# Kernel optimization log

Measured on AMD Instinct MI355X. Metric: run time of the kernel, lower is better.

Reference implementation:

```python
import jax, jax.numpy as jnp
import numpy as np

L_SEG, M_CHEB, MODES1, MODES2 = 4, 8, 16, 16


def _cft(signals, t_coords, f_points, L, M):
    # signals: [N, C, n] real; returns (real, imag) each [N, C, F]
    n = signals.shape[-1]
    seg_len = 1.0 / L
    starts = jnp.linspace(0.0, 1.0, L + 1)[:-1]                      # [L]
    k = jnp.arange(M, dtype=jnp.float32)
    nodes = -jnp.cos((2.0 * k + 1.0) * jnp.pi / (2.0 * M))           # [M]
    T = jnp.cos(k[:, None] * jnp.arccos(nodes)[None, :])             # [M(k), M(m)]
    w_prime = f_points * (2.0 * jnp.pi * (seg_len / 2.0))            # [F]
    angle = nodes[:, None] * w_prime[None, :]                        # [M, F]
    # quad weights (index k is reused as node index m downstream, as in original)
    Wr = (T @ jnp.cos(angle)) * (seg_len / 2.0)                      # [M, F]
    Wi = (T @ (-jnp.sin(angle))) * (seg_len / 2.0)                   # [M, F] (sign = -1, forward)
    # chebyshev sample points for all segments at once
    t_seg = starts[:, None] + (seg_len / 2.0) * (nodes[None, :] + 1.0)   # [L, M]
    right = jnp.clip(jnp.searchsorted(t_coords, t_seg), 0, n - 1)
    left = jnp.clip(right - 1, 0, n - 1)
    tl, tr = t_coords[left], t_coords[right]
    denom = jnp.where(tr - tl < 1e-8, 1.0, tr - tl)
    wr = (t_seg - tl) / denom
    wl = 1.0 - wr
    seg_sig = wl * signals[..., left] + wr * signals[..., right]     # [N, C, L, M]
    Sr = jnp.einsum('nclm,mf->nclf', seg_sig, Wr)
    Si = jnp.einsum('nclm,mf->nclf', seg_sig, Wi)
    phase = -2.0 * jnp.pi * starts[:, None] * f_points[None, :]      # [L, F]
    cr, ci = jnp.cos(phase), jnp.sin(phase)
    real = jnp.sum(Sr * cr - Si * ci, axis=2)
    imag = jnp.sum(Sr * ci + Si * cr, axis=2)
    return real, imag


def _cft2d(x, m1, m2, L, M):
    B, C, H, W = x.shape
    tw = jnp.linspace(0.0, 1.0, W)
    fw = jnp.fft.rfftfreq(W, d=1.0 / W)[:m2].astype(jnp.float32)
    xr = x.transpose(0, 2, 1, 3).reshape(B * H, C, W)
    r, i = _cft(xr, tw, fw, L, M)                                    # [B*H, C, m2]
    r = r.reshape(B, H, C, m2).transpose(0, 2, 1, 3)                 # [B, C, H, m2]
    i = i.reshape(B, H, C, m2).transpose(0, 2, 1, 3)
    th = jnp.linspace(0.0, 1.0, H)
    fh = jnp.fft.fftfreq(H, d=1.0 / H).astype(jnp.float32)
    hidx = np.concatenate([np.arange(0, m1 // 2), np.arange(H - (m1 - m1 // 2), H)])
    fsel = fh[hidx]
    rh = r.transpose(0, 3, 1, 2).reshape(B * m2, C, H)
    ih = i.transpose(0, 3, 1, 2).reshape(B * m2, C, H)
    rr, ri = _cft(rh, th, fsel, L, M)
    ir, ii = _cft(ih, th, fsel, L, M)
    real = (rr - ii).reshape(B, m2, C, m1).transpose(0, 2, 3, 1)     # [B, C, m1, m2]
    imag = (ri + ir).reshape(B, m2, C, m1).transpose(0, 2, 3, 1)
    return real, imag


def setup_inputs() -> dict:
    key = jax.random.key(0)
    ks = jax.random.split(key, 6)
    B, C, O, H, W = 32, 64, 64, 128, 128
    m1, m2 = MODES1, MODES2
    scale = 1.0 / (C * O)
    x = jax.random.normal(ks[0], (B, C, H, W), jnp.float32)
    w1 = scale * jax.random.uniform(ks[1], (C, O, m1, m2, 2), jnp.float32)
    w2 = scale * jax.random.uniform(ks[2], (C, O, m1, m2, 2), jnp.float32)
    d_in = C * (m1 // 4) * (m2 // 4) * 2
    hid = (C + O) * 2
    lin1_w = jax.random.normal(ks[3], (d_in, hid), jnp.float32) * 0.02
    lin1_b = jnp.zeros((hid,), jnp.float32)
    lin2_w = jax.random.normal(ks[4], (hid, O), jnp.float32) * 0.02
    lin2_b = jnp.zeros((O,), jnp.float32)
    return dict(x=x, w1=w1, w2=w2, lin1_w=lin1_w, lin1_b=lin1_b, lin2_w=lin2_w, lin2_b=lin2_b)


def reference(x, w1, w2, lin1_w, lin1_b, lin2_w, lin2_b):
    m1, m2 = MODES1, MODES2
    B, C, H, W = x.shape
    O = w1.shape[1]
    # FNO spectral conv
    xf = jnp.fft.rfft2(x)                                            # [B, C, H, W//2+1]
    w1c = w1[..., 0] + 1j * w1[..., 1]
    w2c = w2[..., 0] + 1j * w2[..., 1]
    out_ft = jnp.zeros((B, O, H, W // 2 + 1), jnp.complex64)
    out_ft = out_ft.at[:, :, :m1, :m2].set(
        jnp.einsum('bixy,ioxy->boxy', xf[:, :, :m1, :m2], w1c))
    out_ft = out_ft.at[:, :, H - m1:, :m2].set(
        jnp.einsum('bixy,ioxy->boxy', xf[:, :, H - m1:, :m2], w2c))
    x_fno = jnp.fft.irfft2(out_ft, s=(H, W))
    # Chebyshev-quadrature CFT correction path
    cr, ci = _cft2d(x, m1 // 4, m2 // 4, L_SEG, M_CHEB)              # [B, C, m1//4, m2//4]
    flat = jnp.stack([cr, ci], axis=-1).reshape(B, -1)               # view_as_real + flatten(1)
    h = jax.nn.gelu(flat @ lin1_w + lin1_b, approximate=False)
    corr = h @ lin2_w + lin2_b                                       # [B, O]
    return x_fno + corr[:, :, None, None]
```

## Files before the change

kernel.cpp:

```cpp
#include <hip/hip_runtime.h>
#include <math.h>

#define PI_F 3.14159265358979323846f
#define TWO_PI_F 6.28318530717958647692f

constexpr int Bn = 32, Cn = 64, On = 64, Hn = 128, Wn = 128;

constexpr size_t WSO_FLAT  = 0;
constexpr size_t WSO_CORR  = 65536;
constexpr size_t WSO_HS    = 67584;
constexpr size_t WSO_BIG   = 81920;
constexpr size_t SZ_QTR    = (size_t)2097152;
constexpr size_t WSO_XF    = WSO_BIG + SZ_QTR;
constexpr size_t WSO_OUTFT = WSO_BIG + 4 * SZ_QTR;

struct Tabs {
  float ktw[128][40];
  float cfth[128][8];
};

constexpr double D_PI = 3.14159265358979323846;

constexpr double d_red(double x) {
  while (x >  D_PI) x -= 2.0 * D_PI;
  while (x < -D_PI) x += 2.0 * D_PI;
  return x;
}
constexpr double d_sin(double x) {
  x = d_red(x);
  double x2 = x * x, t = x, s = x;
  for (int n = 1; n <= 10; n++) { t *= -x2 / (double)((2 * n) * (2 * n + 1)); s += t; }
  return s;
}
constexpr double d_cos(double x) {
  x = d_red(x);
  double x2 = x * x, t = 1.0, s = 1.0;
  for (int n = 1; n <= 10; n++) { t *= -x2 / (double)((2 * n - 1) * (2 * n)); s += t; }
  return s;
}

constexpr Tabs make_tabs() {
  Tabs T{};
  double twc[128] = {}, tws[128] = {};
  for (int r = 0; r < 128; r++) {
    double a = 2.0 * D_PI * (double)r / 128.0;
    twc[r] = d_cos(a); tws[r] = d_sin(a);
  }
  for (int kx = 0; kx < 16; kx++)
    for (int w = 0; w < 128; w++) {
      int r = (kx * w) & 127;
      T.ktw[w][2 * kx]     = (float)twc[r];
      T.ktw[w][2 * kx + 1] = (float)(-tws[r]);
    }
  double node[8] = {}, theta[8] = {};
  for (int m = 0; m < 8; m++) { theta[m] = (2.0 * m + 1.0) * D_PI / 16.0; node[m] = -d_cos(theta[m]); }
  double Tch[8][8] = {};
  for (int k = 0; k < 8; k++)
    for (int m = 0; m < 8; m++) Tch[k][m] = d_cos((double)k * (D_PI - theta[m]));
  int LE[4][8] = {}, RI[4][8] = {};
  float WL[4][8] = {}, WR[4][8] = {};
  for (int l = 0; l < 4; l++)
    for (int m = 0; m < 8; m++) {
      float tseg = (float)(0.25 * (double)l + 0.125 * (node[m] + 1.0));
      int ri = (int)(tseg * 127.0f) - 2; if (ri < 0) ri = 0;
      while (ri < 127 && ((float)ri * (1.0f / 127.0f)) < tseg) ri++;
      int le = ri - 1; if (le < 0) le = 0;
      float tl = (float)le * (1.0f / 127.0f), tr = (float)ri * (1.0f / 127.0f);
      float den = (tr - tl < 1e-8f) ? 1.0f : (tr - tl);
      float wr = (tseg - tl) / den;
      LE[l][m] = le; RI[l][m] = ri; WR[l][m] = wr; WL[l][m] = 1.0f - wr;
    }
  for (int p = 0; p < 2; p++)
    for (int f = 0; f < 4; f++) {
      double fval = (p == 0) ? (double)f
                             : ((f == 0) ? 0.0 : (f == 1) ? 1.0 : (f == 2) ? -2.0 : -1.0);
      double wp = fval * (2.0 * D_PI * 0.125);
      double Wr[8] = {}, Wi[8] = {};
      for (int k = 0; k < 8; k++) {
        double sr = 0.0, si = 0.0;
        for (int m = 0; m < 8; m++) {
          sr += Tch[k][m] * d_cos(node[m] * wp);
          si += Tch[k][m] * (-d_sin(node[m] * wp));
        }
        Wr[k] = sr * 0.125; Wi[k] = si * 0.125;
      }
      for (int l = 0; l < 4; l++) {
        double ph = -2.0 * D_PI * (0.25 * (double)l) * fval;
        double cr = d_cos(ph), ci = d_sin(ph);
        for (int m = 0; m < 8; m++) {
          double coefR = Wr[m] * cr - Wi[m] * ci;
          double coefI = Wr[m] * ci + Wi[m] * cr;
          int le = LE[l][m], ri = RI[l][m];
          if (p == 0) {
            T.ktw[le][32 + f] += (float)(WL[l][m] * coefR);
            T.ktw[le][36 + f] += (float)(WL[l][m] * coefI);
            T.ktw[ri][32 + f] += (float)(WR[l][m] * coefR);
            T.ktw[ri][36 + f] += (float)(WR[l][m] * coefI);
          } else {
            T.cfth[le][f]     += (float)(WL[l][m] * coefR);
            T.cfth[le][4 + f] += (float)(WL[l][m] * coefI);
            T.cfth[ri][f]     += (float)(WR[l][m] * coefR);
            T.cfth[ri][4 + f] += (float)(WR[l][m] * coefI);
          }
        }
      }
    }
  return T;
}

constexpr unsigned short cf2bf(float f) {
  unsigned u = __builtin_bit_cast(unsigned, f);
  u += 0x7FFFu + ((u >> 16) & 1u);
  return (unsigned short)(u >> 16);
}
constexpr float cbf2f(unsigned short h) {
  return __builtin_bit_cast(float, (unsigned)h << 16);
}

struct CfthT { float v[128][8]; };
constexpr CfthT make_cfth() {
  CfthT C{};
  Tabs T = make_tabs();
  for (int h = 0; h < 128; h++)
    for (int q = 0; q < 8; q++) C.v[h][q] = T.cfth[h][q];
  return C;
}
__constant__ CfthT g_cfth = make_cfth();

struct alignas(16) BTab {
  unsigned short v[4][2][3][64][8];
};
constexpr BTab make_btab() {
  BTab B{};
  Tabs T = make_tabs();
  for (int ks = 0; ks < 4; ks++)
    for (int jt = 0; jt < 3; jt++)
      for (int lane = 0; lane < 64; lane++)
        for (int j = 0; j < 8; j++) {
          int col = jt * 16 + (lane & 15);
          int k = ks * 32 + (lane >> 4) * 8 + j;
          float val = (col < 40) ? T.ktw[k][col] : 0.0f;
          unsigned short h = cf2bf(val);
          B.v[ks][0][jt][lane][j] = h;
          B.v[ks][1][jt][lane][j] = cf2bf(val - cbf2f(h));
        }
  return B;
}
__constant__ BTab g_btab = make_btab();

struct alignas(16) TBTab {
  unsigned short v[4][8][2][64][8];
};
constexpr TBTab make_tbtab() {
  TBTab T{};
  double twc[128] = {}, tws[128] = {};
  for (int r = 0; r < 128; r++) {
    double a = 2.0 * D_PI * (double)r / 128.0;
    twc[r] = d_cos(a); tws[r] = d_sin(a);
  }
  for (int mt = 0; mt < 4; mt++)
    for (int ks = 0; ks < 8; ks++)
      for (int lane = 0; lane < 64; lane++)
        for (int js = 0; js < 8; js++) {
          int m = mt * 16 + (lane & 15);
          int j = m & 31, ri = m >> 5;
          int k = ks * 32 + (lane >> 4) * 8 + js;
          int h = k >> 1, u = k & 1;
          int ky = (j < 16) ? j : j + 96;
          int idx = (ky * h) & 127;
          double c = twc[idx], s = tws[idx];
          double val = (ri == 0) ? ((u == 0) ? c : s)
                                 : ((u == 0) ? -s : c);
          float f = (float)val;
          unsigned short hi = cf2bf(f);
          T.v[mt][ks][0][lane][js] = hi;
          T.v[mt][ks][1][lane][js] = cf2bf(f - cbf2f(hi));
        }
  return T;
}
__constant__ TBTab g_tbtab = make_tbtab();

struct alignas(16) W1Tab {
  unsigned short v[16][2][2][64][8];
};
constexpr W1Tab make_w1tab() {
  W1Tab T{};
  double twc[128] = {}, tws[128] = {};
  for (int r = 0; r < 128; r++) {
    double a = 2.0 * D_PI * (double)r / 128.0;
    twc[r] = d_cos(a); tws[r] = d_sin(a);
  }
  for (int mt = 0; mt < 16; mt++)
    for (int ks = 0; ks < 2; ks++)
      for (int lane = 0; lane < 64; lane++)
        for (int j = 0; j < 8; j++) {
          int r = mt * 16 + (lane & 15);
          int k = ks * 32 + (lane >> 4) * 8 + j;
          int jj = k >> 1, u = k & 1;
          int ky = (jj < 16) ? jj : jj + 96;
          int h = r & 127;
          int idx = (ky * h) & 127;
          double c = twc[idx], s = tws[idx];
          double val = (r < 128) ? ((u == 0) ? c : -s)
                                 : ((u == 0) ? s : c);
          float f = (float)(val * (1.0 / 128.0));
          unsigned short hi = cf2bf(f);
          T.v[mt][ks][0][lane][j] = hi;
          T.v[mt][ks][1][lane][j] = cf2bf(f - cbf2f(hi));
        }
  return T;
}
__constant__ W1Tab g_w1tab = make_w1tab();

struct alignas(16) W2Tab {
  unsigned short v[8][2][64][8];
};
constexpr W2Tab make_w2tab() {
  W2Tab T{};
  double twc[128] = {}, tws[128] = {};
  for (int r = 0; r < 128; r++) {
    double a = 2.0 * D_PI * (double)r / 128.0;
    twc[r] = d_cos(a); tws[r] = d_sin(a);
  }
  for (int nt = 0; nt < 8; nt++)
    for (int lane = 0; lane < 64; lane++)
      for (int j = 0; j < 8; j++) {
        int w = nt * 16 + (lane & 15);
        int k = (lane >> 4) * 8 + j;
        int kx = k >> 1, u = k & 1;
        double val;
        if (kx == 0) val = (u == 0) ? 1.0 : 0.0;
        else {
          int idx = (kx * w) & 127;
          val = (u == 0) ? 2.0 * twc[idx] : -2.0 * tws[idx];
        }
        float f = (float)(val * (1.0 / 128.0));
        unsigned short hi = cf2bf(f);
        T.v[nt][0][lane][j] = hi;
        T.v[nt][1][lane][j] = cf2bf(f - cbf2f(hi));
      }
  return T;
}
__constant__ W2Tab g_w2tab = make_w2tab();

typedef __attribute__((ext_vector_type(8))) __bf16 bf16x8;
typedef __attribute__((ext_vector_type(8))) unsigned short ushort8;
typedef __attribute__((ext_vector_type(4))) float f32x4;

__device__ __forceinline__ unsigned short f2bf(float f) {
  return __builtin_bit_cast(unsigned short, (__bf16)f);
}
__device__ __forceinline__ float bf2f(unsigned short h) {
  return (float)__builtin_bit_cast(__bf16, h);
}

__global__ __launch_bounds__(256) void k_fwd(const float* __restrict__ x,
                                             float* __restrict__ xf,
                                             float* __restrict__ flat) {
  __shared__ unsigned xwlp[128][34];
  __shared__ float cftl[128][9];
  __shared__ float cpart[8][33];
  int t = threadIdx.x;
  int lane = t & 63, wid = t >> 6;
  int bc = blockIdx.x;
  const float* xb = x + (size_t)bc * 16384;
  int r = lane & 15, kg = lane >> 4;
  const float* a0 = xb + (wid * 32 + r) * 128 + kg * 8;
  const float* a1 = a0 + 16 * 128;

  float4 xa[16];
  #pragma unroll
  for (int ks = 0; ks < 4; ks++) {
    xa[2 * ks]     = *reinterpret_cast<const float4*>(a0 + ks * 32);
    xa[2 * ks + 1] = *reinterpret_cast<const float4*>(a0 + ks * 32 + 4);
  }
  #pragma unroll
  for (int ks = 0; ks < 4; ks++) {
    xa[8 + 2 * ks]     = *reinterpret_cast<const float4*>(a1 + ks * 32);
    xa[8 + 2 * ks + 1] = *reinterpret_cast<const float4*>(a1 + ks * 32 + 4);
  }

  bf16x8 ahi[2][4], alo[2][4];
  #pragma unroll
  for (int tl = 0; tl < 2; tl++) {
    #pragma unroll
    for (int ks = 0; ks < 4; ks++) {
      const float* p0 = reinterpret_cast<const float*>(&xa[tl * 8 + 2 * ks]);
      const float* p1 = reinterpret_cast<const float*>(&xa[tl * 8 + 2 * ks + 1]);
      ushort8 hu, lu;
      #pragma unroll
      for (int j = 0; j < 8; j++) {
        float v = (j < 4) ? p0[j] : p1[j - 4];
        unsigned short h = f2bf(v);
        hu[j] = h;
        lu[j] = f2bf(v - bf2f(h));
      }
      ahi[tl][ks] = __builtin_bit_cast(bf16x8, hu);
      alo[tl][ks] = __builtin_bit_cast(bf16x8, lu);
    }
  }

  f32x4 acc[2][3];
  #pragma unroll
  for (int tl = 0; tl < 2; tl++)
    #pragma unroll
    for (int jt = 0; jt < 3; jt++) acc[tl][jt] = f32x4{0.f, 0.f, 0.f, 0.f};
  #pragma unroll
  for (int jt = 0; jt < 3; jt++) {
    #pragma unroll
    for (int ks = 0; ks < 4; ks++) {
      bf16x8 bhi = __builtin_bit_cast(bf16x8,
          *reinterpret_cast<const ushort8*>(&g_btab.v[ks][0][jt][lane][0]));
      bf16x8 blo = __builtin_bit_cast(bf16x8,
          *reinterpret_cast<const ushort8*>(&g_btab.v[ks][1][jt][lane][0]));
      acc[0][jt] = __builtin_amdgcn_mfma_f32_16x16x32_bf16(ahi[0][ks], bhi, acc[0][jt], 0, 0, 0);
      acc[1][jt] = __builtin_amdgcn_mfma_f32_16x16x32_bf16(ahi[1][ks], bhi, acc[1][jt], 0, 0, 0);
      acc[0][jt] = __builtin_amdgcn_mfma_f32_16x16x32_bf16(alo[0][ks], bhi, acc[0][jt], 0, 0, 0);
      acc[1][jt] = __builtin_amdgcn_mfma_f32_16x16x32_bf16(alo[1][ks], bhi, acc[1][jt], 0, 0, 0);
      acc[0][jt] = __builtin_amdgcn_mfma_f32_16x16x32_bf16(ahi[0][ks], blo, acc[0][jt], 0, 0, 0);
      acc[1][jt] = __builtin_amdgcn_mfma_f32_16x16x32_bf16(ahi[1][ks], blo, acc[1][jt], 0, 0, 0);
    }
  }
  {
    int col = lane & 15, rq = lane >> 4;
    #pragma unroll
    for (int tl = 0; tl < 2; tl++) {
      int rt = wid * 2 + tl;
      #pragma unroll
      for (int jt = 0; jt < 3; jt++) {
        #pragma unroll
        for (int i = 0; i < 4; i++) {
          int rl = rt * 16 + rq * 4 + i;
          float v = acc[tl][jt][i];
          if (jt < 2) {
            unsigned short hi = f2bf(v);
            unsigned short lo = f2bf(v - bf2f(hi));
            xwlp[rl][jt * 16 + col] = ((unsigned)lo << 16) | (unsigned)hi;
          } else if (col < 8) {
            cftl[rl][col] = v;
          }
        }
      }
    }
  }
  __syncthreads();

  {
    int o = t & 31, seg = t >> 5;
    int f1 = o >> 3, f2 = (o >> 1) & 3, ri = o & 1;
    float acc2 = 0.f;
    #pragma unroll
    for (int hh = 0; hh < 16; hh++) {
      int h = seg * 16 + hh;
      float rr = cftl[h][f2], im = cftl[h][4 + f2];
      float kr = g_cfth.v[h][f1], ki = g_cfth.v[h][4 + f1];
      float e0 = ri ? ki : kr;
      float e1 = ri ? kr : -ki;
      acc2 = fmaf(rr, e0, fmaf(im, e1, acc2));
    }
    cpart[seg][o] = acc2;
  }

  {
    int kx = lane & 15, g = lane >> 4;
    f32x4 accA = {0.f, 0.f, 0.f, 0.f};
    f32x4 accB = {0.f, 0.f, 0.f, 0.f};
    #pragma unroll
    for (int ks2 = 0; ks2 < 4; ks2++) {
      #pragma unroll
      for (int half = 0; half < 2; half++) {
        int ks = half * 4 + ks2;
        int h0 = ks * 16 + g * 4;
        ushort8 bhU, blU;
        #pragma unroll
        for (int rr = 0; rr < 4; rr++) {
          uint2 p = *reinterpret_cast<const uint2*>(&xwlp[h0 + rr][2 * kx]);
          bhU[2 * rr]     = (unsigned short)(p.x & 0xFFFFu);
          blU[2 * rr]     = (unsigned short)(p.x >> 16);
          bhU[2 * rr + 1] = (unsigned short)(p.y & 0xFFFFu);
          blU[2 * rr + 1] = (unsigned short)(p.y >> 16);
        }
        bf16x8 bhi = __builtin_bit_cast(bf16x8, bhU);
        bf16x8 blo = __builtin_bit_cast(bf16x8, blU);
        bf16x8 thi = __builtin_bit_cast(bf16x8,
            *reinterpret_cast<const ushort8*>(&g_tbtab.v[wid][ks][0][lane][0]));
        bf16x8 tlo = __builtin_bit_cast(bf16x8,
            *reinterpret_cast<const ushort8*>(&g_tbtab.v[wid][ks][1][lane][0]));
        f32x4& acc3 = half ? accB : accA;
        acc3 = __builtin_amdgcn_mfma_f32_16x16x32_bf16(thi, bhi, acc3, 0, 0, 0);
        acc3 = __builtin_amdgcn_mfma_f32_16x16x32_bf16(tlo, bhi, acc3, 0, 0, 0);
        acc3 = __builtin_amdgcn_mfma_f32_16x16x32_bf16(thi, blo, acc3, 0, 0, 0);
      }
    }
    f32x4 accS = accA + accB;
    #pragma unroll
    for (int i = 0; i < 4; i++) {
      int m = wid * 16 + (lane >> 4) * 4 + i;
      int j = m & 31, ri = m >> 5;
      xf[((size_t)bc * 32 + j) * 32 + kx * 2 + ri] = accS[i];
    }
  }
  __syncthreads();

  if (t < 32) {
    float s = 0.f;
    #pragma unroll
    for (int seg = 0; seg < 8; seg++) s += cpart[seg][t];
    int b = bc >> 6, c = bc & 63;
    int f1 = t >> 3, f2 = (t >> 1) & 3, ri = t & 1;
    flat[(size_t)b * 2048 + ((c * 4 + f1) * 4 + f2) * 2 + ri] = s;
  }
}

__global__ __launch_bounds__(256) void k_mlp1(const float* __restrict__ flat,
                                              const float* __restrict__ w1,
                                              const float* __restrict__ b1,
                                              float* __restrict__ hs) {
  __shared__ float part[4][64];
  int bid = blockIdx.x;
  int b = bid >> 2, oc = bid & 3;
  int t = threadIdx.x;
  int ol = t & 63, kc = t >> 6;
  int o = oc * 64 + ol;
  const float* fb = flat + (size_t)b * 2048 + kc * 512;
  const float* wb = w1 + (size_t)(kc * 512) * 256 + o;
  float acc = 0.f;
  for (int k = 0; k < 512; k++) acc = fmaf(fb[k], wb[(size_t)k * 256], acc);
  part[kc][ol] = acc;
  __syncthreads();
  if (t < 64) {
    float a = part[0][t] + part[1][t] + part[2][t] + part[3][t] + b1[oc * 64 + t];
    hs[(size_t)b * 256 + oc * 64 + t] = 0.5f * a * (1.0f + erff(a * 0.70710678118654752f));
  }
}

__global__ void k_mlp2(const float* __restrict__ hs,
                       const float* __restrict__ w2,
                       const float* __restrict__ b2,
                       float* __restrict__ corr) {
  int b = blockIdx.x, t = threadIdx.x;
  const float* hb = hs + (size_t)b * 256;
  float acc = b2[t];
  for (int k = 0; k < 256; k++) acc = fmaf(hb[k], w2[(size_t)k * 64 + t], acc);
  corr[(size_t)b * 64 + t] = acc;
}

__global__ __launch_bounds__(256) void k_stageC(const float* __restrict__ xf,
                                                const float* __restrict__ w1,
                                                const float* __restrict__ w2,
                                                float* __restrict__ outft) {
  __shared__ float xfs[64 * 32];
  int bid = blockIdx.x;
  int sw = (bid & 7) * 128 + (bid >> 3);
  int j = sw >> 5, b = sw & 31;
  int t = threadIdx.x;
  #pragma unroll
  for (int k2 = 0; k2 < 4; k2++) {
    int id = t + k2 * 256;
    int c = id >> 4, kxi = id & 15;
    const float2 v = *reinterpret_cast<const float2*>(
        xf + (((size_t)b * 64 + c) * 32 + j) * 32 + kxi * 2);
    reinterpret_cast<float2*>(xfs)[id] = v;
  }
  __syncthreads();
  int kx = t & 15, og = t >> 4;
  const float* wsel = (j < 16) ? w1 : w2;
  int jr = (j < 16) ? j : j - 16;
  float aR[4], aI[4];
  #pragma unroll
  for (int i = 0; i < 4; i++) { aR[i] = 0.f; aI[i] = 0.f; }
  for (int c = 0; c < 64; c++) {
    float xr = xfs[c * 32 + kx * 2], xi = xfs[c * 32 + kx * 2 + 1];
    #pragma unroll
    for (int i = 0; i < 4; i++) {
      int o = og * 4 + i;
      const float2 wv = *reinterpret_cast<const float2*>(
          wsel + ((((size_t)c * 64 + o) * 16 + jr) * 16 + kx) * 2);
      aR[i] = fmaf(xr, wv.x, fmaf(-xi, wv.y, aR[i]));
      aI[i] = fmaf(xr, wv.y, fmaf(xi, wv.x, aI[i]));
    }
  }
  int boff = (j >> 4) * 512 + ((((j >> 2) & 3) << 4) | kx) * 8 + (j & 3) * 2;
  #pragma unroll
  for (int i = 0; i < 4; i++) {
    int o = og * 4 + i;
    float2* dst = reinterpret_cast<float2*>(outft + (size_t)(b * 64 + o) * 1024 + boff);
    *dst = make_float2(aR[i], aI[i]);
  }
}

__global__ __launch_bounds__(256) void k_stageDE(const float* __restrict__ outft,
                                                 const float* __restrict__ corr,
                                                 float* __restrict__ out) {
  __shared__ float Yl[256 * 17];
  int t = threadIdx.x;
  int lane = t & 63, wid = t >> 6;
  int bo = blockIdx.x;
  const float* src = outft + (size_t)bo * 1024;

  bf16x8 shi[2], slo[2];
  #pragma unroll
  for (int ks = 0; ks < 2; ks++) {
    float4 v0 = *reinterpret_cast<const float4*>(src + ks * 512 + lane * 8);
    float4 v1 = *reinterpret_cast<const float4*>(src + ks * 512 + lane * 8 + 4);
    float xv[8] = {v0.x, v0.y, v0.z, v0.w, v1.x, v1.y, v1.z, v1.w};
    ushort8 hu, lu;
    #pragma unroll
    for (int j = 0; j < 8; j++) {
      unsigned short h = f2bf(xv[j]);
      hu[j] = h;
      lu[j] = f2bf(xv[j] - bf2f(h));
    }
    shi[ks] = __builtin_bit_cast(bf16x8, hu);
    slo[ks] = __builtin_bit_cast(bf16x8, lu);
  }

  #pragma unroll
  for (int mtl = 0; mtl < 4; mtl++) {
    int mt = wid * 4 + mtl;
    f32x4 acc = {0.f, 0.f, 0.f, 0.f};
    #pragma unroll
    for (int ks = 0; ks < 2; ks++) {
      bf16x8 whi = __builtin_bit_cast(bf16x8,
          *reinterpret_cast<const ushort8*>(&g_w1tab.v[mt][ks][0][lane][0]));
      bf16x8 wlo = __builtin_bit_cast(bf16x8,
          *reinterpret_cast<const ushort8*>(&g_w1tab.v[mt][ks][1][lane][0]));
      acc = __builtin_amdgcn_mfma_f32_16x16x32_bf16(whi, shi[ks], acc, 0, 0, 0);
      acc = __builtin_amdgcn_mfma_f32_16x16x32_bf16(wlo, shi[ks], acc, 0, 0, 0);
      acc = __builtin_amdgcn_mfma_f32_16x16x32_bf16(whi, slo[ks], acc, 0, 0, 0);
    }
    #pragma unroll
    for (int i = 0; i < 4; i++)
      Yl[(mt * 16 + (lane >> 4) * 4 + i) * 17 + (lane & 15)] = acc[i];
  }
  __syncthreads();

  float corrv = corr[bo];
  float* obase = out + (size_t)bo * 16384;

  #pragma unroll
  for (int mtl = 0; mtl < 2; mtl++) {
    int mt2 = wid * 2 + mtl;
    int h = mt2 * 16 + (lane & 15);
    ushort8 ahiU, aloU;
    #pragma unroll
    for (int j = 0; j < 8; j++) {
      int k = (lane >> 4) * 8 + j;
      float v = Yl[((k & 1) * 128 + h) * 17 + (k >> 1)];
      unsigned short hi = f2bf(v);
      ahiU[j] = hi;
      aloU[j] = f2bf(v - bf2f(hi));
    }
    bf16x8 ahi = __builtin_bit_cast(bf16x8, ahiU);
    bf16x8 alo = __builtin_bit_cast(bf16x8, aloU);
    #pragma unroll
    for (int nt = 0; nt < 8; nt++) {
      bf16x8 bhi = __builtin_bit_cast(bf16x8,
          *reinterpret_cast<const ushort8*>(&g_w2tab.v[nt][0][lane][0]));
      bf16x8 blo = __builtin_bit_cast(bf16x8,
          *reinterpret_cast<const ushort8*>(&g_w2tab.v[nt][1][lane][0]));
      f32x4 acc = {corrv, corrv, corrv, corrv};
      acc = __builtin_amdgcn_mfma_f32_16x16x32_bf16(ahi, bhi, acc, 0, 0, 0);
      acc = __builtin_amdgcn_mfma_f32_16x16x32_bf16(alo, bhi, acc, 0, 0, 0);
      acc = __builtin_amdgcn_mfma_f32_16x16x32_bf16(ahi, blo, acc, 0, 0, 0);
      #pragma unroll
      for (int i = 0; i < 4; i++)
        obase[(mt2 * 16 + (lane >> 4) * 4 + i) * 128 + nt * 16 + (lane & 15)] = acc[i];
    }
  }
}

extern "C" void kernel_launch(void* const* d_in, const int* in_sizes, int n_in,
                              void* d_out, int out_size, void* d_ws, size_t ws_size,
                              hipStream_t stream) {
  const float* x   = (const float*)d_in[0];
  const float* w1  = (const float*)d_in[1];
  const float* w2  = (const float*)d_in[2];
  const float* l1w = (const float*)d_in[3];
  const float* l1b = (const float*)d_in[4];
  const float* l2w = (const float*)d_in[5];
  const float* l2b = (const float*)d_in[6];
  float* out = (float*)d_out;
  float* ws  = (float*)d_ws;

  float* flat  = ws + WSO_FLAT;
  float* corr  = ws + WSO_CORR;
  float* hs    = ws + WSO_HS;
  float* xf    = ws + WSO_XF;
  float* outft = ws + WSO_OUTFT;

  k_fwd<<<dim3(2048), dim3(256), 0, stream>>>(x, xf, flat);
  k_mlp1<<<dim3(128), dim3(256), 0, stream>>>(flat, l1w, l1b, hs);
  k_mlp2<<<dim3(32), dim3(64), 0, stream>>>(hs, l2w, l2b, corr);
  k_stageC<<<dim3(1024), dim3(256), 0, stream>>>(xf, w1, w2, outft);
  k_stageDE<<<dim3(2048), dim3(256), 0, stream>>>(outft, corr, out);
}
```

Baseline: 141.8 us.

## Batch four samples per block in spectral mixing to reuse weight loads

The spectral channel-mixing kernel now handles four batch elements per block instead of one. Each weight value loaded from global memory is reused across the four batches, which cuts weight traffic by four. The grid shrinks from 1024 to 256 blocks and the block-to-mode mapping changes to keep XCD locality. In exchange, register use per thread and shared memory per block both grow, and fewer blocks means lower occupancy and parallelism on a chip with 256 CUs.

```diff
diff --git a/kernel.cpp b/kernel.cpp
--- a/kernel.cpp
+++ b/kernel.cpp
@@ -403,12 +403,12 @@
   __syncthreads();
 
   if (t < 32) {
-    float s = 0.f;
-    #pragma unroll
-    for (int seg = 0; seg < 8; seg++) s += cpart[seg][t];
+    float sum = 0.f;
+    #pragma unroll
+    for (int seg = 0; seg < 8; seg++) sum += cpart[seg][t];
     int b = bc >> 6, c = bc & 63;
     int f1 = t >> 3, f2 = (t >> 1) & 3, ri = t & 1;
-    flat[(size_t)b * 2048 + ((c * 4 + f1) * 4 + f2) * 2 + ri] = s;
+    flat[(size_t)b * 2048 + ((c * 4 + f1) * 4 + f2) * 2 + ri] = sum;
   }
 }
 
@@ -449,43 +449,66 @@
                                                 const float* __restrict__ w1,
                                                 const float* __restrict__ w2,
                                                 float* __restrict__ outft) {
-  __shared__ float xfs[64 * 32];
+  __shared__ float xfs[4][2048];
   int bid = blockIdx.x;
-  int sw = (bid & 7) * 128 + (bid >> 3);
-  int j = sw >> 5, b = sw & 31;
+  int xcd = bid & 7, kk = bid >> 3;
+  int j = xcd * 4 + (kk & 3);
+  int bq = kk >> 2;
+  int b0 = bq * 4;
   int t = threadIdx.x;
-  #pragma unroll
-  for (int k2 = 0; k2 < 4; k2++) {
-    int id = t + k2 * 256;
-    int c = id >> 4, kxi = id & 15;
-    const float2 v = *reinterpret_cast<const float2*>(
-        xf + (((size_t)b * 64 + c) * 32 + j) * 32 + kxi * 2);
-    reinterpret_cast<float2*>(xfs)[id] = v;
+
+  #pragma unroll
+  for (int bb = 0; bb < 4; bb++) {
+    int b = b0 + bb;
+    #pragma unroll
+    for (int k2 = 0; k2 < 4; k2++) {
+      int id = t + k2 * 256;
+      int c = id >> 4, kxi = id & 15;
+      const float2 v = *reinterpret_cast<const float2*>(
+          xf + (((size_t)b * 64 + c) * 32 + j) * 32 + kxi * 2);
+      reinterpret_cast<float2*>(&xfs[bb][0])[id] = v;
+    }
   }
   __syncthreads();
+
   int kx = t & 15, og = t >> 4;
   const float* wsel = (j < 16) ? w1 : w2;
   int jr = (j < 16) ? j : j - 16;
-  float aR[4], aI[4];
-  #pragma unroll
-  for (int i = 0; i < 4; i++) { aR[i] = 0.f; aI[i] = 0.f; }
+  float aR[4][4], aI[4][4];
+  #pragma unroll
+  for (int bb = 0; bb < 4; bb++)
+    #pragma unroll
+    for (int i = 0; i < 4; i++) { aR[bb][i] = 0.f; aI[bb][i] = 0.f; }
+
   for (int c = 0; c < 64; c++) {
-    float xr = xfs[c * 32 + kx * 2], xi = xfs[c * 32 + kx * 2 + 1];
+    float2 wv[4];
     #pragma unroll
     for (int i = 0; i < 4; i++) {
       int o = og * 4 + i;
-      const float2 wv = *reinterpret_cast<const float2*>(
+      wv[i] = *reinterpret_cast<const float2*>(
           wsel + ((((size_t)c * 64 + o) * 16 + jr) * 16 + kx) * 2);
-      aR[i] = fmaf(xr, wv.x, fmaf(-xi, wv.y, aR[i]));
-      aI[i] = fmaf(xr, wv.y, fmaf(xi, wv.x, aI[i]));
-    }
-  }
+    }
+    #pragma unroll
+    for (int bb = 0; bb < 4; bb++) {
+      float xr = xfs[bb][c * 32 + kx * 2], xi = xfs[bb][c * 32 + kx * 2 + 1];
+      #pragma unroll
+      for (int i = 0; i < 4; i++) {
+        aR[bb][i] = fmaf(xr, wv[i].x, fmaf(-xi, wv[i].y, aR[bb][i]));
+        aI[bb][i] = fmaf(xr, wv[i].y, fmaf(xi, wv[i].x, aI[bb][i]));
+      }
+    }
+  }
+
   int boff = (j >> 4) * 512 + ((((j >> 2) & 3) << 4) | kx) * 8 + (j & 3) * 2;
   #pragma unroll
-  for (int i = 0; i < 4; i++) {
-    int o = og * 4 + i;
-    float2* dst = reinterpret_cast<float2*>(outft + (size_t)(b * 64 + o) * 1024 + boff);
-    *dst = make_float2(aR[i], aI[i]);
+  for (int bb = 0; bb < 4; bb++) {
+    int b = b0 + bb;
+    #pragma unroll
+    for (int i = 0; i < 4; i++) {
+      int o = og * 4 + i;
+      float2* dst = reinterpret_cast<float2*>(outft + (size_t)(b * 64 + o) * 1024 + boff);
+      *dst = make_float2(aR[bb][i], aI[bb][i]);
+    }
   }
 }
 
@@ -592,6 +615,6 @@
   k_fwd<<<dim3(2048), dim3(256), 0, stream>>>(x, xf, flat);
   k_mlp1<<<dim3(128), dim3(256), 0, stream>>>(flat, l1w, l1b, hs);
   k_mlp2<<<dim3(32), dim3(64), 0, stream>>>(hs, l2w, l2b, corr);
-  k_stageC<<<dim3(1024), dim3(256), 0, stream>>>(xf, w1, w2, outft);
+  k_stageC<<<dim3(256), dim3(256), 0, stream>>>(xf, w1, w2, outft);
   k_stageDE<<<dim3(2048), dim3(256), 0, stream>>>(outft, corr, out);
 }
```

New measurement: 126.9 us. 1.12x faster.
